# Kernel tuning notes

Measured on AMD Instinct MI355X. Metric: run time of the kernel, lower is better.

Reference implementation:

```python
import jax, jax.numpy as jnp
import numpy as np

B, N, D = 16, 512, 256
PH, UH, UPH = 8, 4, 4          # P_GAT heads, U_GAT heads, UP_GAT heads
P_LAYERS, U_LAYERS = 2, 1
FH, NC = 128, 2                # final hidden, num classes
N_TRAIT = 4


def setup_inputs() -> dict:
    key = jax.random.key(0)
    keys = iter(jax.random.split(key, 64))

    def rn(shape, s=0.05):
        return jax.random.normal(next(keys), shape, dtype=jnp.float32) * s

    inp = {
        "p_mask": jnp.ones((B, N), jnp.float32),
        "feature": rn((B, N, D), 1.0),
        "c_node": rn((B, 1, D), 1.0),
        "pgat_W": rn((D, D)),
        "pgat_attn": rn((PH, 2 * (D // PH))),
    }
    for i in range(1, 5):
        inp[f"up{i}_qw"] = rn((D, D))
        inp[f"up{i}_qb"] = rn((D,))
        inp[f"up{i}_kw"] = rn((D, D))
        inp[f"up{i}_kb"] = rn((D,))
        inp[f"up{i}_ow"] = rn((D, D * UPH))
        inp[f"up{i}_ob"] = rn((D,))
    inp["ugat_W"] = rn((D, D))
    inp["ugat_attn"] = rn((UH, 2 * (D // UH)))
    inp["mlp_w1"] = rn((FH, D))
    inp["mlp_b1"] = rn((FH,))
    inp["mlp_w2"] = rn((FH, FH))
    inp["mlp_b2"] = rn((FH,))
    for i in range(1, 5):
        inp[f"fcf{i}_w"] = rn((NC, FH))
        inp[f"fcf{i}_b"] = rn((NC,))
    return inp


def _mh_gat(feature, W, attn_w, n_head, num_layers, adj=None):
    """Shared math of P_GAT / U_GAT.
    attn(cat([q_i, k_j]))[..., h, h] decomposes into q_i.wq_h + k_j.wk_h,
    identical math to the broadcast-concat-linear-diagonal in the source."""
    Bx, Nx, d = feature.shape
    dh = d // n_head
    wq, wk = attn_w[:, :dh], attn_w[:, dh:]           # [h, dh] each
    for _ in range(num_layers):
        qk = (feature @ W.T).reshape(Bx, Nx, n_head, dh)
        sq = jnp.einsum('bqhd,hd->bqh', qk, wq)
        sk = jnp.einsum('bkhd,hd->bkh', qk, wk)
        scores = jnp.tanh(sq[:, :, None, :] + sk[:, None, :, :])  # [B,q,k,h]
        if adj is not None:
            scores = jnp.where(adj[:, :, :, None] == 0, jnp.float32(-1e-8), scores)
        att = jax.nn.softmax(scores, axis=-2)          # softmax over k
        hid = jnp.tanh(jnp.einsum('bqkh,bkhd->bqhd', att, qk))
        feature = feature + hid.reshape(Bx, Nx, d)
    return feature


def _up_gat(p_mask, p_feat, u_feat, qw, qb, kw, kb, ow, ob):
    """UP_GAT: all heads/layers share params & inputs -> identical heads."""
    d = p_feat.shape[-1]
    q = u_feat @ qw.T + qb                             # [B,1,D]
    k = p_feat @ kw.T + kb                             # [B,Np,D]
    sim = jnp.einsum('bqd,bkd->bqk', q, k) / jnp.sqrt(jnp.float32(d))
    sim = jnp.where(p_mask[:, None, :] == 0, jnp.float32(1e-8), sim)
    att = jax.nn.softmax(sim, axis=2)
    head = att @ p_feat                                # [B,1,D]
    mh = jnp.concatenate([head] * UPH, axis=-1)        # concat of identical heads
    return (mh @ ow.T + ob)[:, 0, :]                   # squeeze(1)


def reference(p_mask, feature, c_node, pgat_W, pgat_attn,
              up1_qw, up1_qb, up1_kw, up1_kb, up1_ow, up1_ob,
              up2_qw, up2_qb, up2_kw, up2_kb, up2_ow, up2_ob,
              up3_qw, up3_qb, up3_kw, up3_kb, up3_ow, up3_ob,
              up4_qw, up4_qb, up4_kw, up4_kb, up4_ow, up4_ob,
              ugat_W, ugat_attn, mlp_w1, mlp_b1, mlp_w2, mlp_b2,
              fcf1_w, fcf1_b, fcf2_w, fcf2_b, fcf3_w, fcf3_b, fcf4_w, fcf4_b):
    Bx = p_mask.shape[0]
    adj = p_mask[:, :, None] * p_mask[:, None, :]      # [B,N,N]
    new_p = _mh_gat(feature, pgat_W, pgat_attn, PH, P_LAYERS, adj=adj)
    new_mask = jnp.concatenate([p_mask, jnp.ones((Bx, 1), p_mask.dtype)], axis=1)
    comb = jnp.concatenate([new_p, c_node], axis=1)    # [B,N+1,D]

    u1 = _up_gat(new_mask, comb, c_node, up1_qw, up1_qb, up1_kw, up1_kb, up1_ow, up1_ob)
    u2 = _up_gat(new_mask, comb, c_node, up2_qw, up2_qb, up2_kw, up2_kb, up2_ow, up2_ob)
    u3 = _up_gat(new_mask, comb, c_node, up3_qw, up3_qb, up3_kw, up3_kb, up3_ow, up3_ob)
    u4 = _up_gat(new_mask, comb, c_node, up4_qw, up4_qb, up4_kw, up4_kb, up4_ow, up4_ob)

    u = jnp.stack([u1, u2, u3, u4], axis=1)            # [B,4,D]
    u = _mh_gat(u, ugat_W, ugat_attn, UH, U_LAYERS, adj=None)

    def mlp(x):  # fcs1..4 share modules in the torch source
        h = jax.nn.relu(x @ mlp_w1.T + mlp_b1)
        return jax.nn.relu(h @ mlp_w2.T + mlp_b2)

    heads = [(fcf1_w, fcf1_b), (fcf2_w, fcf2_b), (fcf3_w, fcf3_b), (fcf4_w, fcf4_b)]
    logits = [mlp(u[:, i]) @ w.T + b for i, (w, b) in enumerate(heads)]
    return jnp.stack(logits, axis=0)                   # [4,B,NC]
```

## Files before the change

kernel.cpp:

```cpp
#include <hip/hip_runtime.h>

constexpr int CB   = 16;
constexpr int CN   = 512;
constexpr int CD   = 256;
constexpr int CPH  = 8;
constexpr int CDH  = 32;
constexpr int CNP1 = 513;
constexpr int CFH  = 128;
constexpr int CNC  = 2;

typedef __bf16 bf16x8 __attribute__((ext_vector_type(8)));
typedef __bf16 bf16x4 __attribute__((ext_vector_type(4)));
typedef float  f32x4  __attribute__((ext_vector_type(4)));

__device__ __forceinline__ float tanh_fast(float x) {
  x = fminf(fmaxf(x, -15.f), 15.f);
  float e = __expf(2.f * x);
  return (e - 1.f) / (e + 1.f);
}

__device__ __forceinline__ float exp2x_clamped(float x) {
  x = fminf(fmaxf(x, -18.f), 18.f);
  return __expf(2.f * x);
}

__global__ __launch_bounds__(256) void prep_wsplit(
    const float* __restrict__ W, bf16x8* __restrict__ wfH, bf16x8* __restrict__ wfL)
{
  const int id = blockIdx.x * 256 + threadIdx.x;
  const int row = id >> 5;
  const int c   = id & 31;
  const float* src = W + (size_t)row * CD + c * 8;
  float4 a0 = *(const float4*)src, a1 = *(const float4*)(src + 4);
  float v[8] = {a0.x, a0.y, a0.z, a0.w, a1.x, a1.y, a1.z, a1.w};
  bf16x8 hi, lo;
#pragma unroll
  for (int j = 0; j < 8; j++) {
    hi[j] = (__bf16)v[j];
    lo[j] = (__bf16)(v[j] - (float)hi[j]);
  }
  const int x = row >> 6, jj = (row >> 4) & 3, lc = row & 15;
  const int s = c >> 2, q = c & 3;
  const int idx = (((x * 8 + s) * 4 + jj) * 4 + q) * 16 + lc;
  wfH[idx] = hi;
  wfL[idx] = lo;
}

__global__ __launch_bounds__(256) void gemm_fused(
    const float* __restrict__ A,
    const bf16x8* __restrict__ wfH, const bf16x8* __restrict__ wfL,
    const float* __restrict__ attnw, __bf16* __restrict__ C,
    float* __restrict__ sqT, float* __restrict__ skT,
    const float* __restrict__ cnode,
    const float* __restrict__ qw0, const float* __restrict__ qb0,
    const float* __restrict__ kw0, const float* __restrict__ kb0,
    const float* __restrict__ ow0,
    const float* __restrict__ qw1, const float* __restrict__ qb1,
    const float* __restrict__ kw1, const float* __restrict__ kb1,
    const float* __restrict__ ow1,
    const float* __restrict__ qw2, const float* __restrict__ qb2,
    const float* __restrict__ kw2, const float* __restrict__ kb2,
    const float* __restrict__ ow2,
    const float* __restrict__ qw3, const float* __restrict__ qb3,
    const float* __restrict__ kw3, const float* __restrict__ kb3,
    const float* __restrict__ ow3,
    float* __restrict__ qt_, float* __restrict__ qkb,
    float* __restrict__ comb, float* __restrict__ head, float* __restrict__ den,
    float* __restrict__ weff)
{
  const int t  = threadIdx.x;

  __shared__ float s_cl[CD];
  __shared__ float s_ql[CD];
  __shared__ float s_red[256];

  if (blockIdx.y >= 128) {
    const int up = blockIdx.x, b = blockIdx.y - 128;
    const float* qw = (up == 0) ? qw0 : (up == 1) ? qw1 : (up == 2) ? qw2 : qw3;
    const float* qb = (up == 0) ? qb0 : (up == 1) ? qb1 : (up == 2) ? qb2 : qb3;
    const float* kw = (up == 0) ? kw0 : (up == 1) ? kw1 : (up == 2) ? kw2 : kw3;
    const float* kb = (up == 0) ? kb0 : (up == 1) ? kb1 : (up == 2) ? kb2 : kb3;
    const float* ow = (up == 0) ? ow0 : (up == 1) ? ow1 : (up == 2) ? ow2 : ow3;
    s_cl[t] = cnode[b * CD + t];
    head[((size_t)b * 4 + up) * CD + t] = 0.f;
    if (t == 0) den[b * 4 + up] = 0.f;

    {
#pragma unroll
      for (int i = 0; i < 4; i++) {
        int idx = t + 256 * i;
        int n = b * 16 + (idx >> 6), e4 = (idx & 63) * 4;
        const float* base = ow + (size_t)n * (4 * CD) + e4;
        float4 w0 = *(const float4*)(base);
        float4 w1 = *(const float4*)(base + CD);
        float4 w2 = *(const float4*)(base + 2 * CD);
        float4 w3 = *(const float4*)(base + 3 * CD);
        float4 o;
        o.x = w0.x + w1.x + w2.x + w3.x;
        o.y = w0.y + w1.y + w2.y + w3.y;
        o.z = w0.z + w1.z + w2.z + w3.z;
        o.w = w0.w + w1.w + w2.w + w3.w;
        *(float4*)(weff + (size_t)up * CD * CD + (size_t)n * CD + e4) = o;
      }
    }
    __syncthreads();
    if (up == 0) comb[((size_t)b * CNP1 + CN) * CD + t] = s_cl[t];
    {
      const float* wr = qw + (size_t)t * CD;
      float a = qb[t];
#pragma unroll 4
      for (int k = 0; k < CD; k += 4) {
        float4 w4 = *(const float4*)(wr + k);
        a += s_cl[k] * w4.x + s_cl[k + 1] * w4.y + s_cl[k + 2] * w4.z + s_cl[k + 3] * w4.w;
      }
      s_ql[t] = a;
    }
    __syncthreads();
    {
      float a0 = 0.f, a1 = 0.f, a2 = 0.f, a3 = 0.f;
#pragma unroll 4
      for (int d = 0; d < CD; d += 4) {
        a0 += s_ql[d]     * kw[(d)     * CD + t];
        a1 += s_ql[d + 1] * kw[(d + 1) * CD + t];
        a2 += s_ql[d + 2] * kw[(d + 2) * CD + t];
        a3 += s_ql[d + 3] * kw[(d + 3) * CD + t];
      }
      qt_[((size_t)up * CB + b) * CD + t] = (a0 + a1) + (a2 + a3);
    }
    s_red[t] = s_ql[t] * kb[t];
    __syncthreads();
    for (int s = 128; s > 0; s >>= 1) { if (t < s) s_red[t] += s_red[t + s]; __syncthreads(); }
    if (t == 0) qkb[up * CB + b] = s_red[0];
    return;
  }

  const int x  = blockIdx.x;
  const int nt = x * 64;
  const int mt = blockIdx.y * 64;
  const int wv = t >> 6, ln = t & 63;
  const int quad = ln >> 4, lc = ln & 15;

  f32x4 acc[4];
#pragma unroll
  for (int j = 0; j < 4; j++)
#pragma unroll
    for (int r = 0; r < 4; r++) acc[j][r] = 0.f;

  const float* ap = A + (size_t)(mt + wv * 16 + lc) * CD + quad * 8;

#pragma unroll 2
  for (int s = 0; s < 8; s++) {
    float4 a0 = *(const float4*)(ap + s * 32);
    float4 a1 = *(const float4*)(ap + s * 32 + 4);
    float av[8] = {a0.x, a0.y, a0.z, a0.w, a1.x, a1.y, a1.z, a1.w};
    bf16x8 ah, al;
#pragma unroll
    for (int j = 0; j < 8; j++) {
      ah[j] = (__bf16)av[j];
      al[j] = (__bf16)(av[j] - (float)ah[j]);
    }
    const int base = ((x * 8 + s) * 16 + quad) * 16 + lc;
#pragma unroll
    for (int j = 0; j < 4; j++) {
      bf16x8 bh = wfH[base + j * 64];
      bf16x8 bl = wfL[base + j * 64];
      acc[j] = __builtin_amdgcn_mfma_f32_16x16x32_bf16(ah, bh, acc[j], 0, 0, 0);
      acc[j] = __builtin_amdgcn_mfma_f32_16x16x32_bf16(ah, bl, acc[j], 0, 0, 0);
      acc[j] = __builtin_amdgcn_mfma_f32_16x16x32_bf16(al, bh, acc[j], 0, 0, 0);
    }
  }
#pragma unroll
  for (int j = 0; j < 4; j++)
#pragma unroll
    for (int r = 0; r < 4; r++)
      C[(size_t)(mt + wv * 16 + quad * 4 + r) * 256 + nt + j * 16 + lc] =
          (__bf16)acc[j][r];

  const int hA = blockIdx.x * 2, hB = hA + 1;
  const float wqa0 = attnw[hA * 64 + lc],      wqa1 = attnw[hA * 64 + 16 + lc];
  const float wka0 = attnw[hA * 64 + 32 + lc], wka1 = attnw[hA * 64 + 48 + lc];
  const float wqb0 = attnw[hB * 64 + lc],      wqb1 = attnw[hB * 64 + 16 + lc];
  const float wkb0 = attnw[hB * 64 + 32 + lc], wkb1 = attnw[hB * 64 + 48 + lc];
  float sqa[4], ska[4], sqb[4], skb[4];
#pragma unroll
  for (int r = 0; r < 4; r++) {
    sqa[r] = acc[0][r] * wqa0 + acc[1][r] * wqa1;
    ska[r] = acc[0][r] * wka0 + acc[1][r] * wka1;
    sqb[r] = acc[2][r] * wqb0 + acc[3][r] * wqb1;
    skb[r] = acc[2][r] * wkb0 + acc[3][r] * wkb1;
  }
#pragma unroll
  for (int m = 1; m <= 8; m <<= 1) {
#pragma unroll
    for (int r = 0; r < 4; r++) {
      sqa[r] += __shfl_xor(sqa[r], m);
      ska[r] += __shfl_xor(ska[r], m);
      sqb[r] += __shfl_xor(sqb[r], m);
      skb[r] += __shfl_xor(skb[r], m);
    }
  }
  if (lc == 0) {
#pragma unroll
    for (int r = 0; r < 4; r++) {
      int gm = mt + wv * 16 + quad * 4 + r;
      int bb = gm >> 9, nn = gm & 511;
      sqT[((size_t)bb * CPH + hA) * CN + nn] = sqa[r];
      skT[((size_t)bb * CPH + hA) * CN + nn] = ska[r];
      sqT[((size_t)bb * CPH + hB) * CN + nn] = sqb[r];
      skT[((size_t)bb * CPH + hB) * CN + nn] = skb[r];
    }
  }
}

__global__ __launch_bounds__(256) void pgat_attn_mfma2(
    const __bf16* __restrict__ qk, const float* __restrict__ sqT,
    const float* __restrict__ skT, const float* __restrict__ pmask,
    const float* __restrict__ fin, float* __restrict__ fout, int outStride)
{
  const int qt = blockIdx.x;
  const int h  = blockIdx.y;
  const int b  = blockIdx.z;
  const int t  = threadIdx.x;
  const int wv = t >> 6;
  const int ln = t & 63;
  const int quad = ln >> 4;
  const int lc   = ln & 15;

  __shared__ __align__(16) __bf16 pbuf[128][72];
  __shared__ __align__(16) __bf16 vbuf[32][72];
  __shared__ float skl[CN];
  __shared__ float ckm[CN];
  __shared__ float sql[128];
  __shared__ float qfm[128];

  for (int i = t; i < CN; i += 256) {
    skl[i] = exp2x_clamped(skT[((size_t)b * CPH + h) * CN + i]);
    ckm[i] = (pmask[b * CN + i] == 0.f) ? 0.f : 1.f;
  }
  if (t < 128) {
    sql[t] = exp2x_clamped(sqT[((size_t)b * CPH + h) * CN + qt * 128 + t]);
    qfm[t] = (pmask[b * CN + qt * 128 + t] == 0.f) ? 0.f : 1.f;
  }

  f32x4 aV0 = {0.f,0.f,0.f,0.f}, aV1 = {0.f,0.f,0.f,0.f}, aD = {0.f,0.f,0.f,0.f};
  f32x4 bV0 = {0.f,0.f,0.f,0.f}, bV1 = {0.f,0.f,0.f,0.f}, bD = {0.f,0.f,0.f,0.f};
  bf16x8 ones;
#pragma unroll
  for (int j = 0; j < 8; j++) ones[j] = (__bf16)1.0f;

  const int qg  = t >> 1;
  const int kb  = (t & 1) * 32;
  const int vkk = t >> 3;
  const int vdq = (t & 7) * 4;

  for (int k0 = 0; k0 < CN; k0 += 64) {
    __syncthreads();
    {
      bf16x4 v0 = *(const bf16x4*)(qk + ((size_t)(b * CN + k0 + vkk)) * CD + h * CDH + vdq);
      bf16x4 v1 = *(const bf16x4*)(qk + ((size_t)(b * CN + k0 + 32 + vkk)) * CD + h * CDH + vdq);
      vbuf[vdq + 0][vkk] = v0[0]; vbuf[vdq + 1][vkk] = v0[1];
      vbuf[vdq + 2][vkk] = v0[2]; vbuf[vdq + 3][vkk] = v0[3];
      vbuf[vdq + 0][32 + vkk] = v1[0]; vbuf[vdq + 1][32 + vkk] = v1[1];
      vbuf[vdq + 2][32 + vkk] = v1[2]; vbuf[vdq + 3][32 + vkk] = v1[3];
    }
    {
      const float tq = sql[qg];
      const float qf = qfm[qg];
#pragma unroll
      for (int g = 0; g < 4; g++) {
        bf16x8 w;
#pragma unroll
        for (int j = 0; j < 8; j++) {
          const int kk = k0 + kb + g * 8 + j;
          float u  = tq * skl[kk];
          float th = (u - 1.f) * __builtin_amdgcn_rcpf(u + 1.f);
          th *= qf * ckm[kk];
          w[j] = (__bf16)__expf(th);
        }
        *(bf16x8*)&pbuf[qg][kb + g * 8] = w;
      }
    }
    __syncthreads();
#pragma unroll
    for (int s = 0; s < 2; s++) {
      bf16x8 b0 = *(const bf16x8*)&vbuf[lc][s * 32 + quad * 8];
      bf16x8 b1 = *(const bf16x8*)&vbuf[16 + lc][s * 32 + quad * 8];
      bf16x8 fa = *(const bf16x8*)&pbuf[wv * 16 + lc][s * 32 + quad * 8];
      bf16x8 fb = *(const bf16x8*)&pbuf[64 + wv * 16 + lc][s * 32 + quad * 8];
      aV0 = __builtin_amdgcn_mfma_f32_16x16x32_bf16(fa, b0, aV0, 0, 0, 0);
      aV1 = __builtin_amdgcn_mfma_f32_16x16x32_bf16(fa, b1, aV1, 0, 0, 0);
      aD  = __builtin_amdgcn_mfma_f32_16x16x32_bf16(fa, ones, aD, 0, 0, 0);
      bV0 = __builtin_amdgcn_mfma_f32_16x16x32_bf16(fb, b0, bV0, 0, 0, 0);
      bV1 = __builtin_amdgcn_mfma_f32_16x16x32_bf16(fb, b1, bV1, 0, 0, 0);
      bD  = __builtin_amdgcn_mfma_f32_16x16x32_bf16(fb, ones, bD, 0, 0, 0);
    }
  }
#pragma unroll
  for (int r = 0; r < 4; r++) {
    const int d0 = h * CDH + lc;
    {
      int q = qt * 128 + wv * 16 + quad * 4 + r;
      float inv = 1.f / aD[r];
      const float* ip = fin + ((size_t)b * CN + q) * CD;
      float*       op = fout + ((size_t)b * outStride + q) * CD;
      op[d0]      = ip[d0]      + tanh_fast(aV0[r] * inv);
      op[d0 + 16] = ip[d0 + 16] + tanh_fast(aV1[r] * inv);
    }
    {
      int q = qt * 128 + 64 + wv * 16 + quad * 4 + r;
      float inv = 1.f / bD[r];
      const float* ip = fin + ((size_t)b * CN + q) * CD;
      float*       op = fout + ((size_t)b * outStride + q) * CD;
      op[d0]      = ip[d0]      + tanh_fast(bV0[r] * inv);
      op[d0 + 16] = ip[d0 + 16] + tanh_fast(bV1[r] * inv);
    }
  }
}


__global__ __launch_bounds__(256) void up_headsim(
    const float* __restrict__ comb, const float* __restrict__ qt,
    const float* __restrict__ qkb, const float* __restrict__ pmask,
    float* __restrict__ head, float* __restrict__ den)
{
  const int b = blockIdx.x, n0 = blockIdx.y * 64, t = threadIdx.x;
  const int up = t >> 6, j = t & 63;
  __shared__ float qtl[4][CD];
  __shared__ float qkbl[4];
  __shared__ float attl[4][64];
  for (int i = t; i < 4 * CD; i += 256)
    qtl[i >> 8][i & 255] = qt[((size_t)(i >> 8) * CB + b) * CD + (i & 255)];
  if (t < 4) qkbl[t] = qkb[t * CB + b];
  __syncthreads();
  {
    const int n = n0 + j;
    float e = 0.f;
    if (n < CNP1) {
      const float* cr = comb + ((size_t)b * CNP1 + n) * CD;
      float p = 0.f;
#pragma unroll 4
      for (int d = 0; d < CD; d += 4) {
        float4 c4 = *(const float4*)(cr + d);
        p += qtl[up][d] * c4.x + qtl[up][d + 1] * c4.y
           + qtl[up][d + 2] * c4.z + qtl[up][d + 3] * c4.w;
      }
      float s = (p + qkbl[up]) * 0.0625f;
      float m = (n < CN) ? pmask[b * CN + n] : 1.f;
      if (m == 0.f) s = 1e-8f;
      e = __expf(s);
    }
    attl[up][j] = e;
  }
  __syncthreads();
  float4 acc = make_float4(0.f, 0.f, 0.f, 0.f);
  const int nmax = min(64, CNP1 - n0);
  for (int jj = 0; jj < nmax; jj++) {
    float a = attl[up][jj];
    float4 c4 = *(const float4*)(comb + ((size_t)b * CNP1 + n0 + jj) * CD + j * 4);
    acc.x += a * c4.x; acc.y += a * c4.y; acc.z += a * c4.z; acc.w += a * c4.w;
  }
  float* hp = head + ((size_t)b * 4 + up) * CD + j * 4;
  atomicAdd(hp + 0, acc.x); atomicAdd(hp + 1, acc.y);
  atomicAdd(hp + 2, acc.z); atomicAdd(hp + 3, acc.w);
  if (j == 0) {
    float s = 0.f;
    for (int jj = 0; jj < 64; jj++) s += attl[up][jj];
    atomicAdd(den + b * 4 + up, s);
  }
}

__global__ __launch_bounds__(256) void up_out_ugat(
    const float* __restrict__ head, const float* __restrict__ den,
    const float* __restrict__ weff,
    const float* __restrict__ ob0, const float* __restrict__ ob1,
    const float* __restrict__ ob2, const float* __restrict__ ob3,
    const float* __restrict__ ugat_W, const float* __restrict__ attnw,
    float* __restrict__ uout, float* __restrict__ uqk, float* __restrict__ sqk)
{
  const int b = blockIdx.x, up = blockIdx.y, t = threadIdx.x;
  const float* ob = (up == 0) ? ob0 : (up == 1) ? ob1 : (up == 2) ? ob2 : ob3;
  __shared__ float hl[CD];
  __shared__ float xl[CD];
  __shared__ float qkl[CD];
  hl[t] = head[((size_t)b * 4 + up) * CD + t] * (1.f / den[b * 4 + up]);
  __syncthreads();
  {
    const float* r0 = weff + (size_t)up * CD * CD + (size_t)t * CD;
    float p0 = 0.f, p1 = 0.f, p2 = 0.f, p3 = 0.f;
#pragma unroll 4
    for (int d = 0; d < CD; d += 16) {
      float4 w0 = *(const float4*)(r0 + d);
      float4 w1 = *(const float4*)(r0 + d + 4);
      float4 w2 = *(const float4*)(r0 + d + 8);
      float4 w3 = *(const float4*)(r0 + d + 12);
      p0 += hl[d +  0] * w0.x + hl[d +  1] * w0.y + hl[d +  2] * w0.z + hl[d +  3] * w0.w;
      p1 += hl[d +  4] * w1.x + hl[d +  5] * w1.y + hl[d +  6] * w1.z + hl[d +  7] * w1.w;
      p2 += hl[d +  8] * w2.x + hl[d +  9] * w2.y + hl[d + 10] * w2.z + hl[d + 11] * w2.w;
      p3 += hl[d + 12] * w3.x + hl[d + 13] * w3.y + hl[d + 14] * w3.z + hl[d + 15] * w3.w;
    }
    float a = ob[t] + ((p0 + p1) + (p2 + p3));
    xl[t] = a;
    uout[((size_t)b * 4 + up) * CD + t] = a;
  }
  __syncthreads();
  {
    const float* wr = ugat_W + (size_t)t * CD;
    float p0 = 0.f, p1 = 0.f, p2 = 0.f, p3 = 0.f;
#pragma unroll 4
    for (int d = 0; d < CD; d += 16) {
      float4 w0 = *(const float4*)(wr + d);
      float4 w1 = *(const float4*)(wr + d + 4);
      float4 w2 = *(const float4*)(wr + d + 8);
      float4 w3 = *(const float4*)(wr + d + 12);
      p0 += xl[d +  0] * w0.x + xl[d +  1] * w0.y + xl[d +  2] * w0.z + xl[d +  3] * w0.w;
      p1 += xl[d +  4] * w1.x + xl[d +  5] * w1.y + xl[d +  6] * w1.z + xl[d +  7] * w1.w;
      p2 += xl[d +  8] * w2.x + xl[d +  9] * w2.y + xl[d + 10] * w2.z + xl[d + 11] * w2.w;
      p3 += xl[d + 12] * w3.x + xl[d + 13] * w3.y + xl[d + 14] * w3.z + xl[d + 15] * w3.w;
    }
    float a = (p0 + p1) + (p2 + p3);
    qkl[t] = a;
    uqk[((size_t)b * 4 + up) * CD + t] = a;
  }
  __syncthreads();
  if (t < 8) {
    const int h = t >> 1, which = t & 1;
    const float* w = attnw + h * 128 + which * 64;
    float s = 0.f;
    for (int j = 0; j < 64; j++) s += qkl[h * 64 + j] * w[j];
    sqk[(((size_t)b * 4 + up) * 4 + h) * 2 + which] = s;
  }
}

__global__ __launch_bounds__(256) void ugat_mlp2(
    const float* __restrict__ u, const float* __restrict__ uqk,
    const float* __restrict__ sqk,
    const float* __restrict__ w1, const float* __restrict__ b1,
    const float* __restrict__ w2, const float* __restrict__ b2,
    const float* __restrict__ f1w, const float* __restrict__ f1b,
    const float* __restrict__ f2w, const float* __restrict__ f2b,
    const float* __restrict__ f3w, const float* __restrict__ f3b,
    const float* __restrict__ f4w, const float* __restrict__ f4b,
    float* __restrict__ out)
{
  const int b = blockIdx.x, trait = blockIdx.y, t = threadIdx.x;
  __shared__ float uq[4][CD];
  __shared__ float sl[4][4], kl[4][4];
  __shared__ float xl[CD];
  __shared__ float h1[CFH];
  __shared__ float h2[CFH];
  for (int i = t; i < 4 * CD; i += 256) uq[i >> 8][i & 255] = uqk[(size_t)b * 4 * CD + i];
  if (t < 16) {
    int node = t >> 2, h = t & 3;
    sl[node][h] = sqk[(((size_t)b * 4 + node) * 4 + h) * 2 + 0];
    kl[node][h] = sqk[(((size_t)b * 4 + node) * 4 + h) * 2 + 1];
  }
  float ur = u[((size_t)b * 4 + trait) * CD + t];
  __syncthreads();
  {
    const int h = t >> 6;
    float e[4]; float ssum = 0.f;
#pragma unroll
    for (int k = 0; k < 4; k++) { e[k] = __expf(tanh_fast(sl[trait][h] + kl[k][h])); ssum += e[k]; }
    float hid = 0.f;
#pragma unroll
    for (int k = 0; k < 4; k++) hid += e[k] * uq[k][t];
    xl[t] = ur + tanh_fast(hid / ssum);
  }
  __syncthreads();
  if (t < CFH) {
    const float* r = w1 + (size_t)t * CD;
    float a = b1[t];
#pragma unroll 4
    for (int k = 0; k < CD; k += 4) {
      float4 v = *(const float4*)(r + k);
      a += xl[k] * v.x + xl[k + 1] * v.y + xl[k + 2] * v.z + xl[k + 3] * v.w;
    }
    h1[t] = fmaxf(a, 0.f);
  }
  __syncthreads();
  if (t < CFH) {
    const float* r = w2 + (size_t)t * CFH;
    float a = b2[t];
#pragma unroll 4
    for (int k = 0; k < CFH; k += 4) {
      float4 v = *(const float4*)(r + k);
      a += h1[k] * v.x + h1[k + 1] * v.y + h1[k + 2] * v.z + h1[k + 3] * v.w;
    }
    h2[t] = fmaxf(a, 0.f);
  }
  __syncthreads();
  if (t < CNC) {
    const float* fw; const float* fb;
    switch (trait) {
      case 0:  fw = f1w; fb = f1b; break;
      case 1:  fw = f2w; fb = f2b; break;
      case 2:  fw = f3w; fb = f3b; break;
      default: fw = f4w; fb = f4b; break;
    }
    const float* r = fw + (size_t)t * CFH;
    float a = fb[t];
    for (int k = 0; k < CFH; k++) a += h2[k] * r[k];
    out[(size_t)trait * (CB * CNC) + b * CNC + t] = a;
  }
}

extern "C" void kernel_launch(void* const* d_in, const int* in_sizes, int n_in,
                              void* d_out, int out_size, void* d_ws, size_t ws_size,
                              hipStream_t stream) {
  (void)in_sizes; (void)n_in; (void)out_size; (void)ws_size;
  const float* pmask    = (const float*)d_in[0];
  const float* feature  = (const float*)d_in[1];
  const float* cnode    = (const float*)d_in[2];
  const float* pgat_W   = (const float*)d_in[3];
  const float* pgat_att = (const float*)d_in[4];
  const float* upw[4][6];
  for (int i = 0; i < 4; i++)
    for (int j = 0; j < 6; j++) upw[i][j] = (const float*)d_in[5 + i * 6 + j];
  const float* ugat_W   = (const float*)d_in[29];
  const float* ugat_att = (const float*)d_in[30];
  const float* mlp_w1 = (const float*)d_in[31];
  const float* mlp_b1 = (const float*)d_in[32];
  const float* mlp_w2 = (const float*)d_in[33];
  const float* mlp_b2 = (const float*)d_in[34];
  const float* fcf[8];
  for (int j = 0; j < 8; j++) fcf[j] = (const float*)d_in[35 + j];

  float* ws = (float*)d_ws;
  size_t o = 0;
  float* ws_qk   = ws + o; o += (size_t)CB * CN * CD;
  float* ws_feat = ws + o; o += (size_t)CB * CN * CD;
  float* ws_comb = ws + o; o += (size_t)CB * CNP1 * CD;
  float* ws_sq   = ws + o; o += (size_t)CB * CPH * CN;
  float* ws_sk   = ws + o; o += (size_t)CB * CPH * CN;
  float* ws_qt   = ws + o; o += (size_t)4 * CB * CD;
  float* ws_qkb  = ws + o; o += 4 * CB;
  float* ws_den  = ws + o; o += CB * 4;
  float* ws_head = ws + o; o += (size_t)CB * 4 * CD;
  float* ws_u    = ws + o; o += (size_t)CB * 4 * CD;
  float* ws_uqk  = ws + o; o += (size_t)CB * 4 * CD;
  float* ws_sqk  = ws + o; o += (size_t)CB * 4 * 4 * 2;
  float* ws_weff = ws + o; o += (size_t)4 * CD * CD;
  float* ws_wfh  = ws + o; o += (size_t)CD * CD / 2;
  float* ws_wfl  = ws + o; o += (size_t)CD * CD / 2;
  __bf16* qk16 = (__bf16*)ws_qk;
  bf16x8* wfH = (bf16x8*)ws_wfh;
  bf16x8* wfL = (bf16x8*)ws_wfl;

  const dim3 gemmGrid1(CD / 64, (CB * CN) / 64 + 16);
  const dim3 gemmGrid2(CD / 64, (CB * CN) / 64);
  const dim3 attnGrid(CN / 128, CPH, CB);

  prep_wsplit<<<dim3(32), 256, 0, stream>>>(pgat_W, wfH, wfL);

  gemm_fused<<<gemmGrid1, 256, 0, stream>>>(feature, wfH, wfL, pgat_att, qk16, ws_sq, ws_sk,
      cnode,
      upw[0][0], upw[0][1], upw[0][2], upw[0][3], upw[0][4],
      upw[1][0], upw[1][1], upw[1][2], upw[1][3], upw[1][4],
      upw[2][0], upw[2][1], upw[2][2], upw[2][3], upw[2][4],
      upw[3][0], upw[3][1], upw[3][2], upw[3][3], upw[3][4],
      ws_qt, ws_qkb, ws_comb, ws_head, ws_den, ws_weff);
  pgat_attn_mfma2<<<attnGrid, 256, 0, stream>>>(qk16, ws_sq, ws_sk, pmask, feature, ws_feat, CN);
  gemm_fused<<<gemmGrid2, 256, 0, stream>>>(ws_feat, wfH, wfL, pgat_att, qk16, ws_sq, ws_sk,
      cnode,
      upw[0][0], upw[0][1], upw[0][2], upw[0][3], upw[0][4],
      upw[1][0], upw[1][1], upw[1][2], upw[1][3], upw[1][4],
      upw[2][0], upw[2][1], upw[2][2], upw[2][3], upw[2][4],
      upw[3][0], upw[3][1], upw[3][2], upw[3][3], upw[3][4],
      ws_qt, ws_qkb, ws_comb, ws_head, ws_den, ws_weff);
  pgat_attn_mfma2<<<attnGrid, 256, 0, stream>>>(qk16, ws_sq, ws_sk, pmask, ws_feat, ws_comb, CNP1);

  up_headsim<<<dim3(CB, (CNP1 + 63) / 64), 256, 0, stream>>>(ws_comb, ws_qt, ws_qkb, pmask,
                                                             ws_head, ws_den);
  up_out_ugat<<<dim3(CB, 4), 256, 0, stream>>>(ws_head, ws_den, ws_weff,
      upw[0][5], upw[1][5], upw[2][5], upw[3][5],
      ugat_W, ugat_att, ws_u, ws_uqk, ws_sqk);

  ugat_mlp2<<<dim3(CB, 4), 256, 0, stream>>>(ws_u, ws_uqk, ws_sqk,
                                             mlp_w1, mlp_b1, mlp_w2, mlp_b2,
                                             fcf[0], fcf[1], fcf[2], fcf[3],
                                             fcf[4], fcf[5], fcf[6], fcf[7],
                                             (float*)d_out);
}
```

Baseline: 267.7 us.

## Fuse P_GAT projection GEMM with attention into one per-layer kernel

Merges the projection GEMM and the attention kernel into a single `pgat_layer` kernel. Each block (query half, head, batch) computes the 32-column head slice of the projection for all 512 rows directly into LDS, along with the q/k attention scalars, then runs the attention over that slice. This removes the bf16 qk buffer and the sq/sk buffers in global memory and halves the number of launches per layer. In exchange, the projection for each head is computed twice (once per query half), LDS use grows to roughly 64KB per block, and the grid drops to 256 attention blocks, which lowers occupancy.

```diff
diff --git a/kernel.cpp b/kernel.cpp
--- a/kernel.cpp
+++ b/kernel.cpp
@@ -46,11 +46,11 @@
   wfL[idx] = lo;
 }
 
-__global__ __launch_bounds__(256) void gemm_fused(
+__global__ __launch_bounds__(256) void pgat_layer(
     const float* __restrict__ A,
     const bf16x8* __restrict__ wfH, const bf16x8* __restrict__ wfL,
-    const float* __restrict__ attnw, __bf16* __restrict__ C,
-    float* __restrict__ sqT, float* __restrict__ skT,
+    const float* __restrict__ attnw, const float* __restrict__ pmask,
+    float* __restrict__ fout, int outStride,
     const float* __restrict__ cnode,
     const float* __restrict__ qw0, const float* __restrict__ qb0,
     const float* __restrict__ kw0, const float* __restrict__ kb0,
@@ -68,14 +68,21 @@
     float* __restrict__ comb, float* __restrict__ head, float* __restrict__ den,
     float* __restrict__ weff)
 {
-  const int t  = threadIdx.x;
-
+  const int t = threadIdx.x;
+
+  __shared__ __align__(16) __bf16 vslice[32][520];
+  __shared__ __align__(16) __bf16 pbuf[128][72];
+  __shared__ float skl[CN];
+  __shared__ float sqlf[CN];
+  __shared__ float cmask[CN];
+  __shared__ float sq_raw[CN];
+  __shared__ float sk_raw[CN];
   __shared__ float s_cl[CD];
   __shared__ float s_ql[CD];
   __shared__ float s_red[256];
 
-  if (blockIdx.y >= 128) {
-    const int up = blockIdx.x, b = blockIdx.y - 128;
+  if (blockIdx.z >= 16) {
+    const int up = blockIdx.z - 16, b = blockIdx.x + 2 * blockIdx.y;
     const float* qw = (up == 0) ? qw0 : (up == 1) ? qw1 : (up == 2) ? qw2 : qw3;
     const float* qb = (up == 0) ? qb0 : (up == 1) ? qb1 : (up == 2) ? qb2 : qb3;
     const float* kw = (up == 0) ? kw0 : (up == 1) ? kw1 : (up == 2) ? kw2 : kw3;
@@ -84,7 +91,6 @@
     s_cl[t] = cnode[b * CD + t];
     head[((size_t)b * 4 + up) * CD + t] = 0.f;
     if (t == 0) den[b * 4 + up] = 0.f;
-
     {
 #pragma unroll
       for (int i = 0; i < 4; i++) {
@@ -134,185 +140,148 @@
     return;
   }
 
-  const int x  = blockIdx.x;
-  const int nt = x * 64;
-  const int mt = blockIdx.y * 64;
+  const int qh = blockIdx.x, h = blockIdx.y, b = blockIdx.z;
   const int wv = t >> 6, ln = t & 63;
   const int quad = ln >> 4, lc = ln & 15;
 
-  f32x4 acc[4];
-#pragma unroll
-  for (int j = 0; j < 4; j++)
-#pragma unroll
-    for (int r = 0; r < 4; r++) acc[j][r] = 0.f;
-
-  const float* ap = A + (size_t)(mt + wv * 16 + lc) * CD + quad * 8;
-
-#pragma unroll 2
-  for (int s = 0; s < 8; s++) {
-    float4 a0 = *(const float4*)(ap + s * 32);
-    float4 a1 = *(const float4*)(ap + s * 32 + 4);
-    float av[8] = {a0.x, a0.y, a0.z, a0.w, a1.x, a1.y, a1.z, a1.w};
-    bf16x8 ah, al;
-#pragma unroll
-    for (int j = 0; j < 8; j++) {
-      ah[j] = (__bf16)av[j];
-      al[j] = (__bf16)(av[j] - (float)ah[j]);
-    }
-    const int base = ((x * 8 + s) * 16 + quad) * 16 + lc;
-#pragma unroll
-    for (int j = 0; j < 4; j++) {
-      bf16x8 bh = wfH[base + j * 64];
-      bf16x8 bl = wfL[base + j * 64];
-      acc[j] = __builtin_amdgcn_mfma_f32_16x16x32_bf16(ah, bh, acc[j], 0, 0, 0);
-      acc[j] = __builtin_amdgcn_mfma_f32_16x16x32_bf16(ah, bl, acc[j], 0, 0, 0);
-      acc[j] = __builtin_amdgcn_mfma_f32_16x16x32_bf16(al, bh, acc[j], 0, 0, 0);
-    }
-  }
-#pragma unroll
-  for (int j = 0; j < 4; j++)
-#pragma unroll
-    for (int r = 0; r < 4; r++)
-      C[(size_t)(mt + wv * 16 + quad * 4 + r) * 256 + nt + j * 16 + lc] =
-          (__bf16)acc[j][r];
-
-  const int hA = blockIdx.x * 2, hB = hA + 1;
-  const float wqa0 = attnw[hA * 64 + lc],      wqa1 = attnw[hA * 64 + 16 + lc];
-  const float wka0 = attnw[hA * 64 + 32 + lc], wka1 = attnw[hA * 64 + 48 + lc];
-  const float wqb0 = attnw[hB * 64 + lc],      wqb1 = attnw[hB * 64 + 16 + lc];
-  const float wkb0 = attnw[hB * 64 + 32 + lc], wkb1 = attnw[hB * 64 + 48 + lc];
-  float sqa[4], ska[4], sqb[4], skb[4];
-#pragma unroll
-  for (int r = 0; r < 4; r++) {
-    sqa[r] = acc[0][r] * wqa0 + acc[1][r] * wqa1;
-    ska[r] = acc[0][r] * wka0 + acc[1][r] * wka1;
-    sqb[r] = acc[2][r] * wqb0 + acc[3][r] * wqb1;
-    skb[r] = acc[2][r] * wkb0 + acc[3][r] * wkb1;
-  }
-#pragma unroll
-  for (int m = 1; m <= 8; m <<= 1) {
+  {
+    const int x = h >> 1, jbase = (h & 1) * 2;
+    f32x4 acc[8][2];
+#pragma unroll
+    for (int m = 0; m < 8; m++)
+#pragma unroll
+      for (int jj = 0; jj < 2; jj++)
+#pragma unroll
+        for (int r = 0; r < 4; r++) acc[m][jj][r] = 0.f;
+
+    const float* arow = A + ((size_t)b * CN + wv * 128 + lc) * CD + quad * 8;
+#pragma unroll 1
+    for (int s = 0; s < 8; s++) {
+      const int fi = (((x * 8 + s) * 4 + jbase) * 4 + quad) * 16 + lc;
+      bf16x8 bh0 = wfH[fi],      bl0 = wfL[fi];
+      bf16x8 bh1 = wfH[fi + 64], bl1 = wfL[fi + 64];
+#pragma unroll
+      for (int m = 0; m < 8; m++) {
+        const float* ap = arow + (size_t)m * 16 * CD + s * 32;
+        float4 a0 = *(const float4*)ap, a1 = *(const float4*)(ap + 4);
+        float av[8] = {a0.x, a0.y, a0.z, a0.w, a1.x, a1.y, a1.z, a1.w};
+        bf16x8 ah, al;
+#pragma unroll
+        for (int j = 0; j < 8; j++) {
+          ah[j] = (__bf16)av[j];
+          al[j] = (__bf16)(av[j] - (float)ah[j]);
+        }
+        acc[m][0] = __builtin_amdgcn_mfma_f32_16x16x32_bf16(ah, bh0, acc[m][0], 0, 0, 0);
+        acc[m][0] = __builtin_amdgcn_mfma_f32_16x16x32_bf16(ah, bl0, acc[m][0], 0, 0, 0);
+        acc[m][0] = __builtin_amdgcn_mfma_f32_16x16x32_bf16(al, bh0, acc[m][0], 0, 0, 0);
+        acc[m][1] = __builtin_amdgcn_mfma_f32_16x16x32_bf16(ah, bh1, acc[m][1], 0, 0, 0);
+        acc[m][1] = __builtin_amdgcn_mfma_f32_16x16x32_bf16(ah, bl1, acc[m][1], 0, 0, 0);
+        acc[m][1] = __builtin_amdgcn_mfma_f32_16x16x32_bf16(al, bh1, acc[m][1], 0, 0, 0);
+      }
+    }
+
+    const float wq0 = attnw[h * 64 + lc],      wq1 = attnw[h * 64 + 16 + lc];
+    const float wk0 = attnw[h * 64 + 32 + lc], wk1 = attnw[h * 64 + 48 + lc];
+#pragma unroll
+    for (int m = 0; m < 8; m++) {
+      const int row0 = wv * 128 + m * 16 + quad * 4;
+      float sqv[4], skv[4];
+#pragma unroll
+      for (int r = 0; r < 4; r++) {
+        vslice[lc][row0 + r]      = (__bf16)acc[m][0][r];
+        vslice[16 + lc][row0 + r] = (__bf16)acc[m][1][r];
+        sqv[r] = acc[m][0][r] * wq0 + acc[m][1][r] * wq1;
+        skv[r] = acc[m][0][r] * wk0 + acc[m][1][r] * wk1;
+      }
+#pragma unroll
+      for (int mm = 1; mm <= 8; mm <<= 1) {
+#pragma unroll
+        for (int r = 0; r < 4; r++) {
+          sqv[r] += __shfl_xor(sqv[r], mm);
+          skv[r] += __shfl_xor(skv[r], mm);
+        }
+      }
+      if (lc == 0) {
+#pragma unroll
+        for (int r = 0; r < 4; r++) {
+          sq_raw[row0 + r] = sqv[r];
+          sk_raw[row0 + r] = skv[r];
+        }
+      }
+    }
+  }
+  __syncthreads();
+  for (int i = t; i < CN; i += 256) {
+    skl[i]   = exp2x_clamped(sk_raw[i]);
+    sqlf[i]  = exp2x_clamped(sq_raw[i]);
+    cmask[i] = (pmask[b * CN + i] == 0.f) ? 0.f : 1.f;
+  }
+
+  const int qg = t >> 1;
+  const int kb = (t & 1) * 32;
+  bf16x8 ones;
+#pragma unroll
+  for (int j = 0; j < 8; j++) ones[j] = (__bf16)1.0f;
+
+#pragma unroll 1
+  for (int qc = 0; qc < 2; qc++) {
+    const int qbase = qh * 256 + qc * 128;
+    f32x4 aV0 = {0.f,0.f,0.f,0.f}, aV1 = {0.f,0.f,0.f,0.f}, aD = {0.f,0.f,0.f,0.f};
+    f32x4 bV0 = {0.f,0.f,0.f,0.f}, bV1 = {0.f,0.f,0.f,0.f}, bD = {0.f,0.f,0.f,0.f};
+
+    for (int k0 = 0; k0 < CN; k0 += 64) {
+      __syncthreads();
+      {
+        const float tq = sqlf[qbase + qg];
+        const float qf = cmask[qbase + qg];
+#pragma unroll
+        for (int g = 0; g < 4; g++) {
+          bf16x8 w;
+#pragma unroll
+          for (int j = 0; j < 8; j++) {
+            const int kk = k0 + kb + g * 8 + j;
+            float u  = tq * skl[kk];
+            float th = (u - 1.f) * __builtin_amdgcn_rcpf(u + 1.f);
+            th *= qf * cmask[kk];
+            w[j] = (__bf16)__expf(th);
+          }
+          *(bf16x8*)&pbuf[qg][kb + g * 8] = w;
+        }
+      }
+      __syncthreads();
+#pragma unroll
+      for (int s = 0; s < 2; s++) {
+        bf16x8 b0 = *(const bf16x8*)&vslice[lc][k0 + s * 32 + quad * 8];
+        bf16x8 b1 = *(const bf16x8*)&vslice[16 + lc][k0 + s * 32 + quad * 8];
+        bf16x8 fa = *(const bf16x8*)&pbuf[wv * 16 + lc][s * 32 + quad * 8];
+        bf16x8 fb = *(const bf16x8*)&pbuf[64 + wv * 16 + lc][s * 32 + quad * 8];
+        aV0 = __builtin_amdgcn_mfma_f32_16x16x32_bf16(fa, b0, aV0, 0, 0, 0);
+        aV1 = __builtin_amdgcn_mfma_f32_16x16x32_bf16(fa, b1, aV1, 0, 0, 0);
+        aD  = __builtin_amdgcn_mfma_f32_16x16x32_bf16(fa, ones, aD, 0, 0, 0);
+        bV0 = __builtin_amdgcn_mfma_f32_16x16x32_bf16(fb, b0, bV0, 0, 0, 0);
+        bV1 = __builtin_amdgcn_mfma_f32_16x16x32_bf16(fb, b1, bV1, 0, 0, 0);
+        bD  = __builtin_amdgcn_mfma_f32_16x16x32_bf16(fb, ones, bD, 0, 0, 0);
+      }
+    }
 #pragma unroll
     for (int r = 0; r < 4; r++) {
-      sqa[r] += __shfl_xor(sqa[r], m);
-      ska[r] += __shfl_xor(ska[r], m);
-      sqb[r] += __shfl_xor(sqb[r], m);
-      skb[r] += __shfl_xor(skb[r], m);
-    }
-  }
-  if (lc == 0) {
-#pragma unroll
-    for (int r = 0; r < 4; r++) {
-      int gm = mt + wv * 16 + quad * 4 + r;
-      int bb = gm >> 9, nn = gm & 511;
-      sqT[((size_t)bb * CPH + hA) * CN + nn] = sqa[r];
-      skT[((size_t)bb * CPH + hA) * CN + nn] = ska[r];
-      sqT[((size_t)bb * CPH + hB) * CN + nn] = sqb[r];
-      skT[((size_t)bb * CPH + hB) * CN + nn] = skb[r];
-    }
-  }
-}
-
-__global__ __launch_bounds__(256) void pgat_attn_mfma2(
-    const __bf16* __restrict__ qk, const float* __restrict__ sqT,
-    const float* __restrict__ skT, const float* __restrict__ pmask,
-    const float* __restrict__ fin, float* __restrict__ fout, int outStride)
-{
-  const int qt = blockIdx.x;
-  const int h  = blockIdx.y;
-  const int b  = blockIdx.z;
-  const int t  = threadIdx.x;
-  const int wv = t >> 6;
-  const int ln = t & 63;
-  const int quad = ln >> 4;
-  const int lc   = ln & 15;
-
-  __shared__ __align__(16) __bf16 pbuf[128][72];
-  __shared__ __align__(16) __bf16 vbuf[32][72];
-  __shared__ float skl[CN];
-  __shared__ float ckm[CN];
-  __shared__ float sql[128];
-  __shared__ float qfm[128];
-
-  for (int i = t; i < CN; i += 256) {
-    skl[i] = exp2x_clamped(skT[((size_t)b * CPH + h) * CN + i]);
-    ckm[i] = (pmask[b * CN + i] == 0.f) ? 0.f : 1.f;
-  }
-  if (t < 128) {
-    sql[t] = exp2x_clamped(sqT[((size_t)b * CPH + h) * CN + qt * 128 + t]);
-    qfm[t] = (pmask[b * CN + qt * 128 + t] == 0.f) ? 0.f : 1.f;
-  }
-
-  f32x4 aV0 = {0.f,0.f,0.f,0.f}, aV1 = {0.f,0.f,0.f,0.f}, aD = {0.f,0.f,0.f,0.f};
-  f32x4 bV0 = {0.f,0.f,0.f,0.f}, bV1 = {0.f,0.f,0.f,0.f}, bD = {0.f,0.f,0.f,0.f};
-  bf16x8 ones;
-#pragma unroll
-  for (int j = 0; j < 8; j++) ones[j] = (__bf16)1.0f;
-
-  const int qg  = t >> 1;
-  const int kb  = (t & 1) * 32;
-  const int vkk = t >> 3;
-  const int vdq = (t & 7) * 4;
-
-  for (int k0 = 0; k0 < CN; k0 += 64) {
-    __syncthreads();
-    {
-      bf16x4 v0 = *(const bf16x4*)(qk + ((size_t)(b * CN + k0 + vkk)) * CD + h * CDH + vdq);
-      bf16x4 v1 = *(const bf16x4*)(qk + ((size_t)(b * CN + k0 + 32 + vkk)) * CD + h * CDH + vdq);
-      vbuf[vdq + 0][vkk] = v0[0]; vbuf[vdq + 1][vkk] = v0[1];
-      vbuf[vdq + 2][vkk] = v0[2]; vbuf[vdq + 3][vkk] = v0[3];
-      vbuf[vdq + 0][32 + vkk] = v1[0]; vbuf[vdq + 1][32 + vkk] = v1[1];
-      vbuf[vdq + 2][32 + vkk] = v1[2]; vbuf[vdq + 3][32 + vkk] = v1[3];
-    }
-    {
-      const float tq = sql[qg];
-      const float qf = qfm[qg];
-#pragma unroll
-      for (int g = 0; g < 4; g++) {
-        bf16x8 w;
-#pragma unroll
-        for (int j = 0; j < 8; j++) {
-          const int kk = k0 + kb + g * 8 + j;
-          float u  = tq * skl[kk];
-          float th = (u - 1.f) * __builtin_amdgcn_rcpf(u + 1.f);
-          th *= qf * ckm[kk];
-          w[j] = (__bf16)__expf(th);
-        }
-        *(bf16x8*)&pbuf[qg][kb + g * 8] = w;
-      }
-    }
-    __syncthreads();
-#pragma unroll
-    for (int s = 0; s < 2; s++) {
-      bf16x8 b0 = *(const bf16x8*)&vbuf[lc][s * 32 + quad * 8];
-      bf16x8 b1 = *(const bf16x8*)&vbuf[16 + lc][s * 32 + quad * 8];
-      bf16x8 fa = *(const bf16x8*)&pbuf[wv * 16 + lc][s * 32 + quad * 8];
-      bf16x8 fb = *(const bf16x8*)&pbuf[64 + wv * 16 + lc][s * 32 + quad * 8];
-      aV0 = __builtin_amdgcn_mfma_f32_16x16x32_bf16(fa, b0, aV0, 0, 0, 0);
-      aV1 = __builtin_amdgcn_mfma_f32_16x16x32_bf16(fa, b1, aV1, 0, 0, 0);
-      aD  = __builtin_amdgcn_mfma_f32_16x16x32_bf16(fa, ones, aD, 0, 0, 0);
-      bV0 = __builtin_amdgcn_mfma_f32_16x16x32_bf16(fb, b0, bV0, 0, 0, 0);
-      bV1 = __builtin_amdgcn_mfma_f32_16x16x32_bf16(fb, b1, bV1, 0, 0, 0);
-      bD  = __builtin_amdgcn_mfma_f32_16x16x32_bf16(fb, ones, bD, 0, 0, 0);
-    }
-  }
-#pragma unroll
-  for (int r = 0; r < 4; r++) {
-    const int d0 = h * CDH + lc;
-    {
-      int q = qt * 128 + wv * 16 + quad * 4 + r;
-      float inv = 1.f / aD[r];
-      const float* ip = fin + ((size_t)b * CN + q) * CD;
-      float*       op = fout + ((size_t)b * outStride + q) * CD;
-      op[d0]      = ip[d0]      + tanh_fast(aV0[r] * inv);
-      op[d0 + 16] = ip[d0 + 16] + tanh_fast(aV1[r] * inv);
-    }
-    {
-      int q = qt * 128 + 64 + wv * 16 + quad * 4 + r;
-      float inv = 1.f / bD[r];
-      const float* ip = fin + ((size_t)b * CN + q) * CD;
-      float*       op = fout + ((size_t)b * outStride + q) * CD;
-      op[d0]      = ip[d0]      + tanh_fast(bV0[r] * inv);
-      op[d0 + 16] = ip[d0 + 16] + tanh_fast(bV1[r] * inv);
+      const int d0 = h * CDH + lc;
+      {
+        int q = qbase + wv * 16 + quad * 4 + r;
+        float inv = 1.f / aD[r];
+        const float* ip = A + ((size_t)b * CN + q) * CD;
+        float*       op = fout + ((size_t)b * outStride + q) * CD;
+        op[d0]      = ip[d0]      + tanh_fast(aV0[r] * inv);
+        op[d0 + 16] = ip[d0 + 16] + tanh_fast(aV1[r] * inv);
+      }
+      {
+        int q = qbase + 64 + wv * 16 + quad * 4 + r;
+        float inv = 1.f / bD[r];
+        const float* ip = A + ((size_t)b * CN + q) * CD;
+        float*       op = fout + ((size_t)b * outStride + q) * CD;
+        op[d0]      = ip[d0]      + tanh_fast(bV0[r] * inv);
+        op[d0 + 16] = ip[d0 + 16] + tanh_fast(bV1[r] * inv);
+      }
     }
   }
 }
@@ -527,11 +496,8 @@
 
   float* ws = (float*)d_ws;
   size_t o = 0;
-  float* ws_qk   = ws + o; o += (size_t)CB * CN * CD;
   float* ws_feat = ws + o; o += (size_t)CB * CN * CD;
   float* ws_comb = ws + o; o += (size_t)CB * CNP1 * CD;
-  float* ws_sq   = ws + o; o += (size_t)CB * CPH * CN;
-  float* ws_sk   = ws + o; o += (size_t)CB * CPH * CN;
   float* ws_qt   = ws + o; o += (size_t)4 * CB * CD;
   float* ws_qkb  = ws + o; o += 4 * CB;
   float* ws_den  = ws + o; o += CB * 4;
@@ -542,32 +508,30 @@
   float* ws_weff = ws + o; o += (size_t)4 * CD * CD;
   float* ws_wfh  = ws + o; o += (size_t)CD * CD / 2;
   float* ws_wfl  = ws + o; o += (size_t)CD * CD / 2;
-  __bf16* qk16 = (__bf16*)ws_qk;
   bf16x8* wfH = (bf16x8*)ws_wfh;
   bf16x8* wfL = (bf16x8*)ws_wfl;
 
-  const dim3 gemmGrid1(CD / 64, (CB * CN) / 64 + 16);
-  const dim3 gemmGrid2(CD / 64, (CB * CN) / 64);
-  const dim3 attnGrid(CN / 128, CPH, CB);
+  const dim3 fusedGrid1(2, CPH, CB + 4);
+  const dim3 fusedGrid2(2, CPH, CB);
 
   prep_wsplit<<<dim3(32), 256, 0, stream>>>(pgat_W, wfH, wfL);
 
-  gemm_fused<<<gemmGrid1, 256, 0, stream>>>(feature, wfH, wfL, pgat_att, qk16, ws_sq, ws_sk,
+  pgat_layer<<<fusedGrid1, 256, 0, stream>>>(feature, wfH, wfL, pgat_att, pmask,
+      ws_feat, CN,
       cnode,
       upw[0][0], upw[0][1], upw[0][2], upw[0][3], upw[0][4],
       upw[1][0], upw[1][1], upw[1][2], upw[1][3], upw[1][4],
       upw[2][0], upw[2][1], upw[2][2], upw[2][3], upw[2][4],
       upw[3][0], upw[3][1], upw[3][2], upw[3][3], upw[3][4],
       ws_qt, ws_qkb, ws_comb, ws_head, ws_den, ws_weff);
-  pgat_attn_mfma2<<<attnGrid, 256, 0, stream>>>(qk16, ws_sq, ws_sk, pmask, feature, ws_feat, CN);
-  gemm_fused<<<gemmGrid2, 256, 0, stream>>>(ws_feat, wfH, wfL, pgat_att, qk16, ws_sq, ws_sk,
+  pgat_layer<<<fusedGrid2, 256, 0, stream>>>(ws_feat, wfH, wfL, pgat_att, pmask,
+      ws_comb, CNP1,
       cnode,
       upw[0][0], upw[0][1], upw[0][2], upw[0][3], upw[0][4],
       upw[1][0], upw[1][1], upw[1][2], upw[1][3], upw[1][4],
       upw[2][0], upw[2][1], upw[2][2], upw[2][3], upw[2][4],
       upw[3][0], upw[3][1], upw[3][2], upw[3][3], upw[3][4],
       ws_qt, ws_qkb, ws_comb, ws_head, ws_den, ws_weff);
-  pgat_attn_mfma2<<<attnGrid, 256, 0, stream>>>(qk16, ws_sq, ws_sk, pmask, ws_feat, ws_comb, CNP1);
 
   up_headsim<<<dim3(CB, (CNP1 + 63) / 64), 256, 0, stream>>>(ws_comb, ws_qt, ws_qkb, pmask,
                                                              ws_head, ws_den);
```

New measurement: 294.6 us. 10.0% more time.

## Preload full V slice to LDS and compute probabilities in registers

Applied to the files above, without the earlier changes.

Rewrites the P_GAT attention kernel so each block loads the whole transposed V slice for its (batch, head) into shared memory once. Each wave then builds its attention-weight fragment directly in registers and feeds it to MFMA, with no per-tile LDS staging or barriers inside the k loop. Query tiles shrink from 128 to 64, which doubles the grid. The cost is that every block reloads the full V slice, so redundant global and LDS traffic grows, and the larger shared-memory footprint may limit occupancy.

```diff
diff --git a/kernel.cpp b/kernel.cpp
--- a/kernel.cpp
+++ b/kernel.cpp
@@ -84,7 +84,6 @@
     s_cl[t] = cnode[b * CD + t];
     head[((size_t)b * 4 + up) * CD + t] = 0.f;
     if (t == 0) den[b * 4 + up] = 0.f;
-
     {
 #pragma unroll
       for (int i = 0; i < 4; i++) {
@@ -212,7 +211,7 @@
   }
 }
 
-__global__ __launch_bounds__(256) void pgat_attn_mfma2(
+__global__ __launch_bounds__(256) void pgat_attn3(
     const __bf16* __restrict__ qk, const float* __restrict__ sqT,
     const float* __restrict__ skT, const float* __restrict__ pmask,
     const float* __restrict__ fin, float* __restrict__ fout, int outStride)
@@ -221,99 +220,63 @@
   const int h  = blockIdx.y;
   const int b  = blockIdx.z;
   const int t  = threadIdx.x;
-  const int wv = t >> 6;
-  const int ln = t & 63;
-  const int quad = ln >> 4;
-  const int lc   = ln & 15;
-
-  __shared__ __align__(16) __bf16 pbuf[128][72];
-  __shared__ __align__(16) __bf16 vbuf[32][72];
+  const int wv = t >> 6, ln = t & 63;
+  const int quad = ln >> 4, lc = ln & 15;
+
+  __shared__ __align__(16) __bf16 vslice[32][520];
   __shared__ float skl[CN];
   __shared__ float ckm[CN];
-  __shared__ float sql[128];
-  __shared__ float qfm[128];
+  __shared__ float sql64[64];
 
   for (int i = t; i < CN; i += 256) {
     skl[i] = exp2x_clamped(skT[((size_t)b * CPH + h) * CN + i]);
     ckm[i] = (pmask[b * CN + i] == 0.f) ? 0.f : 1.f;
   }
-  if (t < 128) {
-    sql[t] = exp2x_clamped(sqT[((size_t)b * CPH + h) * CN + qt * 128 + t]);
-    qfm[t] = (pmask[b * CN + qt * 128 + t] == 0.f) ? 0.f : 1.f;
-  }
-
-  f32x4 aV0 = {0.f,0.f,0.f,0.f}, aV1 = {0.f,0.f,0.f,0.f}, aD = {0.f,0.f,0.f,0.f};
-  f32x4 bV0 = {0.f,0.f,0.f,0.f}, bV1 = {0.f,0.f,0.f,0.f}, bD = {0.f,0.f,0.f,0.f};
+  if (t < 64) sql64[t] = exp2x_clamped(sqT[((size_t)b * CPH + h) * CN + qt * 64 + t]);
+  for (int i = t; i < CN * 4; i += 256) {
+    const int k = i >> 2, dq = (i & 3) * 8;
+    bf16x8 v = *(const bf16x8*)(qk + ((size_t)(b * CN + k)) * CD + h * CDH + dq);
+#pragma unroll
+    for (int j = 0; j < 8; j++) vslice[dq + j][k] = v[j];
+  }
+  __syncthreads();
+
+  const int q0 = qt * 64 + wv * 16;
+  const float tq = sql64[wv * 16 + lc];
+  const float qf = ckm[q0 + lc];
+
+  f32x4 V0 = {0.f,0.f,0.f,0.f}, V1 = {0.f,0.f,0.f,0.f}, Dn = {0.f,0.f,0.f,0.f};
   bf16x8 ones;
 #pragma unroll
   for (int j = 0; j < 8; j++) ones[j] = (__bf16)1.0f;
 
-  const int qg  = t >> 1;
-  const int kb  = (t & 1) * 32;
-  const int vkk = t >> 3;
-  const int vdq = (t & 7) * 4;
-
-  for (int k0 = 0; k0 < CN; k0 += 64) {
-    __syncthreads();
-    {
-      bf16x4 v0 = *(const bf16x4*)(qk + ((size_t)(b * CN + k0 + vkk)) * CD + h * CDH + vdq);
-      bf16x4 v1 = *(const bf16x4*)(qk + ((size_t)(b * CN + k0 + 32 + vkk)) * CD + h * CDH + vdq);
-      vbuf[vdq + 0][vkk] = v0[0]; vbuf[vdq + 1][vkk] = v0[1];
-      vbuf[vdq + 2][vkk] = v0[2]; vbuf[vdq + 3][vkk] = v0[3];
-      vbuf[vdq + 0][32 + vkk] = v1[0]; vbuf[vdq + 1][32 + vkk] = v1[1];
-      vbuf[vdq + 2][32 + vkk] = v1[2]; vbuf[vdq + 3][32 + vkk] = v1[3];
-    }
-    {
-      const float tq = sql[qg];
-      const float qf = qfm[qg];
-#pragma unroll
-      for (int g = 0; g < 4; g++) {
-        bf16x8 w;
-#pragma unroll
-        for (int j = 0; j < 8; j++) {
-          const int kk = k0 + kb + g * 8 + j;
-          float u  = tq * skl[kk];
-          float th = (u - 1.f) * __builtin_amdgcn_rcpf(u + 1.f);
-          th *= qf * ckm[kk];
-          w[j] = (__bf16)__expf(th);
-        }
-        *(bf16x8*)&pbuf[qg][kb + g * 8] = w;
-      }
-    }
-    __syncthreads();
-#pragma unroll
-    for (int s = 0; s < 2; s++) {
-      bf16x8 b0 = *(const bf16x8*)&vbuf[lc][s * 32 + quad * 8];
-      bf16x8 b1 = *(const bf16x8*)&vbuf[16 + lc][s * 32 + quad * 8];
-      bf16x8 fa = *(const bf16x8*)&pbuf[wv * 16 + lc][s * 32 + quad * 8];
-      bf16x8 fb = *(const bf16x8*)&pbuf[64 + wv * 16 + lc][s * 32 + quad * 8];
-      aV0 = __builtin_amdgcn_mfma_f32_16x16x32_bf16(fa, b0, aV0, 0, 0, 0);
-      aV1 = __builtin_amdgcn_mfma_f32_16x16x32_bf16(fa, b1, aV1, 0, 0, 0);
-      aD  = __builtin_amdgcn_mfma_f32_16x16x32_bf16(fa, ones, aD, 0, 0, 0);
-      bV0 = __builtin_amdgcn_mfma_f32_16x16x32_bf16(fb, b0, bV0, 0, 0, 0);
-      bV1 = __builtin_amdgcn_mfma_f32_16x16x32_bf16(fb, b1, bV1, 0, 0, 0);
-      bD  = __builtin_amdgcn_mfma_f32_16x16x32_bf16(fb, ones, bD, 0, 0, 0);
-    }
-  }
+#pragma unroll 2
+  for (int k0 = 0; k0 < CN; k0 += 32) {
+    bf16x8 fa;
+#pragma unroll
+    for (int j = 0; j < 8; j++) {
+      const int kk = k0 + quad * 8 + j;
+      float u  = tq * skl[kk];
+      float th = (u - 1.f) * __builtin_amdgcn_rcpf(u + 1.f);
+      th *= qf * ckm[kk];
+      fa[j] = (__bf16)__expf(th);
+    }
+    bf16x8 b0 = *(const bf16x8*)&vslice[lc][k0 + quad * 8];
+    bf16x8 b1 = *(const bf16x8*)&vslice[16 + lc][k0 + quad * 8];
+    V0 = __builtin_amdgcn_mfma_f32_16x16x32_bf16(fa, b0, V0, 0, 0, 0);
+    V1 = __builtin_amdgcn_mfma_f32_16x16x32_bf16(fa, b1, V1, 0, 0, 0);
+    Dn = __builtin_amdgcn_mfma_f32_16x16x32_bf16(fa, ones, Dn, 0, 0, 0);
+  }
+
+  const int d0 = h * CDH + lc;
 #pragma unroll
   for (int r = 0; r < 4; r++) {
-    const int d0 = h * CDH + lc;
-    {
-      int q = qt * 128 + wv * 16 + quad * 4 + r;
-      float inv = 1.f / aD[r];
-      const float* ip = fin + ((size_t)b * CN + q) * CD;
-      float*       op = fout + ((size_t)b * outStride + q) * CD;
-      op[d0]      = ip[d0]      + tanh_fast(aV0[r] * inv);
-      op[d0 + 16] = ip[d0 + 16] + tanh_fast(aV1[r] * inv);
-    }
-    {
-      int q = qt * 128 + 64 + wv * 16 + quad * 4 + r;
-      float inv = 1.f / bD[r];
-      const float* ip = fin + ((size_t)b * CN + q) * CD;
-      float*       op = fout + ((size_t)b * outStride + q) * CD;
-      op[d0]      = ip[d0]      + tanh_fast(bV0[r] * inv);
-      op[d0 + 16] = ip[d0 + 16] + tanh_fast(bV1[r] * inv);
-    }
+    const int q = q0 + quad * 4 + r;
+    float inv = 1.f / Dn[r];
+    const float* ip = fin + ((size_t)b * CN + q) * CD;
+    float*       op = fout + ((size_t)b * outStride + q) * CD;
+    op[d0]      = ip[d0]      + tanh_fast(V0[r] * inv);
+    op[d0 + 16] = ip[d0 + 16] + tanh_fast(V1[r] * inv);
   }
 }
 
@@ -548,7 +511,7 @@
 
   const dim3 gemmGrid1(CD / 64, (CB * CN) / 64 + 16);
   const dim3 gemmGrid2(CD / 64, (CB * CN) / 64);
-  const dim3 attnGrid(CN / 128, CPH, CB);
+  const dim3 attnGrid(CN / 64, CPH, CB);
 
   prep_wsplit<<<dim3(32), 256, 0, stream>>>(pgat_W, wfH, wfL);
 
@@ -559,7 +522,7 @@
       upw[2][0], upw[2][1], upw[2][2], upw[2][3], upw[2][4],
       upw[3][0], upw[3][1], upw[3][2], upw[3][3], upw[3][4],
       ws_qt, ws_qkb, ws_comb, ws_head, ws_den, ws_weff);
-  pgat_attn_mfma2<<<attnGrid, 256, 0, stream>>>(qk16, ws_sq, ws_sk, pmask, feature, ws_feat, CN);
+  pgat_attn3<<<attnGrid, 256, 0, stream>>>(qk16, ws_sq, ws_sk, pmask, feature, ws_feat, CN);
   gemm_fused<<<gemmGrid2, 256, 0, stream>>>(ws_feat, wfH, wfL, pgat_att, qk16, ws_sq, ws_sk,
       cnode,
       upw[0][0], upw[0][1], upw[0][2], upw[0][3], upw[0][4],
@@ -567,7 +530,7 @@
       upw[2][0], upw[2][1], upw[2][2], upw[2][3], upw[2][4],
       upw[3][0], upw[3][1], upw[3][2], upw[3][3], upw[3][4],
       ws_qt, ws_qkb, ws_comb, ws_head, ws_den, ws_weff);
-  pgat_attn_mfma2<<<attnGrid, 256, 0, stream>>>(qk16, ws_sq, ws_sk, pmask, ws_feat, ws_comb, CNP1);
+  pgat_attn3<<<attnGrid, 256, 0, stream>>>(qk16, ws_sq, ws_sk, pmask, ws_feat, ws_comb, CNP1);
 
   up_headsim<<<dim3(CB, (CNP1 + 63) / 64), 256, 0, stream>>>(ws_comb, ws_qt, ws_qkb, pmask,
                                                              ws_head, ws_den);
```

Result: no change. 268.1 us (+0.2%).
